# Kernel optimization log

Hardware: AMD Instinct MI355X
Metric: run time of the kernel (lower is better)

## Reference

```python
import jax, jax.numpy as jnp
import numpy as np

B, F, ND, NE = 1024, 1024, 256, 256

def setup_inputs() -> dict:
    key = jax.random.key(0)
    k1, k2, k3 = jax.random.split(key, 3)
    x = jax.random.normal(k1, (B, F), dtype=jnp.float32)
    # xavier-uniform-like init scale for (F+1, units)
    lim_d = float(np.sqrt(6.0 / (F + 1 + ND)))
    lim_e = float(np.sqrt(6.0 / (F + 1 + NE)))
    dilations = jax.random.uniform(k2, (F + 1, ND), minval=-lim_d, maxval=lim_d, dtype=jnp.float32)
    erosions = jax.random.uniform(k3, (F + 1, NE), minval=-lim_e, maxval=lim_e, dtype=jnp.float32)
    return {"x": x, "dilations": dilations, "erosions": erosions}

def reference(x, dilations, erosions):
    b = x.shape[0]
    # append a zero 'bias' feature -> (b, F+1)
    xb = jnp.concatenate([x, jnp.zeros((b, 1), dtype=x.dtype)], axis=1)
    # tropical matmuls: max-plus (dilation), min-minus (erosion)
    dilated = jnp.max(xb[:, :, None] + dilations[None, :, :], axis=1)   # (b, ND)
    eroded = jnp.min(xb[:, :, None] - erosions[None, :, :], axis=1)     # (b, NE)
    return jnp.concatenate([eroded, dilated], axis=1)
```

## Files before the change

### kernel.cpp

```cpp
#include <hip/hip_runtime.h>
#include <math.h>

#define BB   1024
#define FF   1024
#define NOUT 512
#define NW   256
#define BT   128
#define NT   64
#define KT   32

__global__ __launch_bounds__(256, 2) void trop_main(
    const float* __restrict__ x,
    const float* __restrict__ dil,
    const float* __restrict__ ero,
    float* __restrict__ dst,
    int ks, int ch, int direct)
{
    const int bx = blockIdx.x;
    const int by = blockIdx.y;
    const int bz = blockIdx.z;
    const bool is_ero = (bx < (NW / NT));
    const float* __restrict__ w = is_ero ? ero : dil;
    const int c0w = is_ero ? bx * NT : bx * NT - NW;
    const int r0 = by * BT;
    const float sgn = is_ero ? -1.0f : 1.0f;

    __shared__ float lds_x[KT][BT];
    __shared__ float lds_w[KT][NT];

    const int tid = threadIdx.x;
    const int cg = tid & 7;
    const int rg = tid >> 3;

    float acc[4][8];
#pragma unroll
    for (int i = 0; i < 4; ++i)
#pragma unroll
        for (int j = 0; j < 8; ++j) acc[i][j] = -INFINITY;

    const int fstart = bz * ch;
    const int nchunk = ch / KT;

    for (int kc = 0; kc < nchunk; ++kc) {
        const int fb = fstart + kc * KT;

#pragma unroll
        for (int it = 0; it < 4; ++it) {
            const int tt = tid + it * 256;
            const int r = tt & 127;
            const int g = tt >> 7;
            const float4 v = *(const float4*)(x + (size_t)(r0 + r) * FF + fb + g * 4);
            lds_x[g * 4 + 0][r] = sgn * v.x;
            lds_x[g * 4 + 1][r] = sgn * v.y;
            lds_x[g * 4 + 2][r] = sgn * v.z;
            lds_x[g * 4 + 3][r] = sgn * v.w;
        }
#pragma unroll
        for (int it = 0; it < 2; ++it) {
            const int tt = tid + it * 256;
            const int f = tt >> 4;
            const int c4 = tt & 15;
            *(float4*)&lds_w[f][c4 * 4] =
                *(const float4*)(w + (size_t)(fb + f) * NW + c0w + c4 * 4);
        }
        __syncthreads();

#pragma unroll
        for (int ff = 0; ff < KT; ff += 2) {
            const float4 x0 = *(const float4*)&lds_x[ff][rg << 2];
            const float4 x1 = *(const float4*)&lds_x[ff + 1][rg << 2];
            const float4 wa0 = *(const float4*)&lds_w[ff][cg << 3];
            const float4 wb0 = *(const float4*)&lds_w[ff][(cg << 3) + 4];
            const float4 wa1 = *(const float4*)&lds_w[ff + 1][cg << 3];
            const float4 wb1 = *(const float4*)&lds_w[ff + 1][(cg << 3) + 4];
            const float xr0[4] = {x0.x, x0.y, x0.z, x0.w};
            const float xr1[4] = {x1.x, x1.y, x1.z, x1.w};
            const float wc0[8] = {wa0.x, wa0.y, wa0.z, wa0.w, wb0.x, wb0.y, wb0.z, wb0.w};
            const float wc1[8] = {wa1.x, wa1.y, wa1.z, wa1.w, wb1.x, wb1.y, wb1.z, wb1.w};
#pragma unroll
            for (int i = 0; i < 4; ++i)
#pragma unroll
                for (int j = 0; j < 8; ++j) {
                    acc[i][j] = fmaxf(acc[i][j],
                                      fmaxf(xr0[i] + wc0[j], xr1[i] + wc1[j]));
                }
        }
        __syncthreads();
    }

    if (bz == ks - 1) {
        const float4 ba = *(const float4*)(w + (size_t)FF * NW + c0w + (cg << 3));
        const float4 bb = *(const float4*)(w + (size_t)FF * NW + c0w + (cg << 3) + 4);
        const float bc[8] = {ba.x, ba.y, ba.z, ba.w, bb.x, bb.y, bb.z, bb.w};
#pragma unroll
        for (int i = 0; i < 4; ++i)
#pragma unroll
            for (int j = 0; j < 8; ++j) acc[i][j] = fmaxf(acc[i][j], bc[j]);
    }

    float* base = direct ? dst : dst + (size_t)bz * (BB * NOUT);
    const int cglob = bx * NT + (cg << 3);
#pragma unroll
    for (int i = 0; i < 4; ++i) {
        const int row = r0 + (rg << 2) + i;
        float4 v0, v1;
        v0.x = sgn * acc[i][0]; v0.y = sgn * acc[i][1];
        v0.z = sgn * acc[i][2]; v0.w = sgn * acc[i][3];
        v1.x = sgn * acc[i][4]; v1.y = sgn * acc[i][5];
        v1.z = sgn * acc[i][6]; v1.w = sgn * acc[i][7];
        *(float4*)(base + (size_t)row * NOUT + cglob) = v0;
        *(float4*)(base + (size_t)row * NOUT + cglob + 4) = v1;
    }
}

__global__ __launch_bounds__(256) void trop_combine(
    const float* __restrict__ ws, float* __restrict__ out, int ks)
{
    const int i4 = blockIdx.x * blockDim.x + threadIdx.x;
    const int col4 = (i4 << 2) & (NOUT - 1);
    const bool ero = col4 < NW;
    const int stride4 = BB * NOUT / 4;
    float4 v = ((const float4*)ws)[i4];
    for (int z = 1; z < ks; ++z) {
        const float4 u = ((const float4*)ws)[(size_t)z * stride4 + i4];
        if (ero) {
            v.x = fminf(v.x, u.x); v.y = fminf(v.y, u.y);
            v.z = fminf(v.z, u.z); v.w = fminf(v.w, u.w);
        } else {
            v.x = fmaxf(v.x, u.x); v.y = fmaxf(v.y, u.y);
            v.z = fmaxf(v.z, u.z); v.w = fmaxf(v.w, u.w);
        }
    }
    ((float4*)out)[i4] = v;
}

extern "C" void kernel_launch(void* const* d_in, const int* in_sizes, int n_in,
                              void* d_out, int out_size, void* d_ws, size_t ws_size,
                              hipStream_t stream) {
    const float* x = (const float*)d_in[0];
    const float* dil = (const float*)d_in[1];
    const float* ero = (const float*)d_in[2];
    float* out = (float*)d_out;

    const size_t outbytes = (size_t)BB * NOUT * sizeof(float);
    int ks = 1;
    if (ws_size >= 8 * outbytes) ks = 8;
    else if (ws_size >= 4 * outbytes) ks = 4;
    else if (ws_size >= 2 * outbytes) ks = 2;

    if (ks > 1) {
        dim3 grid(NOUT / NT, BB / BT, ks);
        trop_main<<<grid, 256, 0, stream>>>(x, dil, ero, (float*)d_ws, ks, FF / ks, 0);
        const int n4 = BB * NOUT / 4;
        trop_combine<<<n4 / 256, 256, 0, stream>>>((const float*)d_ws, out, ks);
    } else {
        dim3 grid(NOUT / NT, BB / BT, 1);
        trop_main<<<grid, 256, 0, stream>>>(x, dil, ero, out, 1, FF, 1);
    }
}
```

Baseline: 91.02 us.

## Double-buffer LDS tiles with register prefetch and template erosion/dilation paths

Adds double-buffered shared-memory tiles: the global loads for the next K chunk go into registers before computing the current chunk and are written to the other buffer afterward, so only one barrier is needed per chunk. The sign multiplication on x is removed by templating the core on erosion vs dilation, computing w - x directly for erosion. This doubles LDS use to about 48KB per block and raises register pressure from the prefetch registers, which may hurt occupancy at 2 blocks per CU.

```diff
diff --git a/kernel.cpp b/kernel.cpp
--- a/kernel.cpp
+++ b/kernel.cpp
@@ -1,36 +1,30 @@
 #include <hip/hip_runtime.h>
 #include <math.h>
 
-#define BB   1024
-#define FF   1024
-#define NOUT 512
-#define NW   256
-#define BT   128
-#define NT   64
-#define KT   32
+#define BB    1024
+#define FF    1024
+#define NOUT  512
+#define NW    256
+#define BT    128
+#define NT    64
+#define KT    32
 
-__global__ __launch_bounds__(256, 2) void trop_main(
+template<bool ERO>
+__device__ __forceinline__ void core(
+    float (* __restrict__ lx)[KT][BT],
+    float (* __restrict__ lw)[KT][NT],
     const float* __restrict__ x,
-    const float* __restrict__ dil,
-    const float* __restrict__ ero,
+    const float* __restrict__ w,
     float* __restrict__ dst,
-    int ks, int ch, int direct)
+    const int c0w, const int ks, const int ch)
 {
-    const int bx = blockIdx.x;
-    const int by = blockIdx.y;
-    const int bz = blockIdx.z;
-    const bool is_ero = (bx < (NW / NT));
-    const float* __restrict__ w = is_ero ? ero : dil;
-    const int c0w = is_ero ? bx * NT : bx * NT - NW;
-    const int r0 = by * BT;
-    const float sgn = is_ero ? -1.0f : 1.0f;
-
-    __shared__ float lds_x[KT][BT];
-    __shared__ float lds_w[KT][NT];
-
     const int tid = threadIdx.x;
-    const int cg = tid & 7;
-    const int rg = tid >> 3;
+    const int cg  = tid & 7;
+    const int rg  = tid >> 3;
+    const int r0  = blockIdx.y * BT;
+    const int bz  = blockIdx.z;
+    const int fstart = bz * ch;
+    const int nchunk = ch / KT;
 
     float acc[4][8];
 #pragma unroll
@@ -38,41 +32,52 @@
 #pragma unroll
         for (int j = 0; j < 8; ++j) acc[i][j] = -INFINITY;
 
-    const int fstart = bz * ch;
-    const int nchunk = ch / KT;
+    float4 xs[4], ws2[2];
 
-    for (int kc = 0; kc < nchunk; ++kc) {
-        const int fb = fstart + kc * KT;
-
+    auto g_load = [&](int fb) {
 #pragma unroll
         for (int it = 0; it < 4; ++it) {
             const int tt = tid + it * 256;
-            const int r = tt & 127;
-            const int g = tt >> 7;
-            const float4 v = *(const float4*)(x + (size_t)(r0 + r) * FF + fb + g * 4);
-            lds_x[g * 4 + 0][r] = sgn * v.x;
-            lds_x[g * 4 + 1][r] = sgn * v.y;
-            lds_x[g * 4 + 2][r] = sgn * v.z;
-            lds_x[g * 4 + 3][r] = sgn * v.w;
+            const int r  = tt & 127;
+            const int g  = tt >> 7;
+            xs[it] = *(const float4*)(x + (size_t)(r0 + r) * FF + fb + g * 4);
         }
 #pragma unroll
         for (int it = 0; it < 2; ++it) {
             const int tt = tid + it * 256;
-            const int f = tt >> 4;
+            const int f  = tt >> 4;
             const int c4 = tt & 15;
-            *(float4*)&lds_w[f][c4 * 4] =
-                *(const float4*)(w + (size_t)(fb + f) * NW + c0w + c4 * 4);
+            ws2[it] = *(const float4*)(w + (size_t)(fb + f) * NW + c0w + c4 * 4);
         }
-        __syncthreads();
-
+    };
+    auto s_write = [&](int b) {
+#pragma unroll
+        for (int it = 0; it < 4; ++it) {
+            const int tt = tid + it * 256;
+            const int r  = tt & 127;
+            const int g  = tt >> 7;
+            lx[b][g * 4 + 0][r] = xs[it].x;
+            lx[b][g * 4 + 1][r] = xs[it].y;
+            lx[b][g * 4 + 2][r] = xs[it].z;
+            lx[b][g * 4 + 3][r] = xs[it].w;
+        }
+#pragma unroll
+        for (int it = 0; it < 2; ++it) {
+            const int tt = tid + it * 256;
+            const int f  = tt >> 4;
+            const int c4 = tt & 15;
+            *(float4*)&lw[b][f][c4 * 4] = ws2[it];
+        }
+    };
+    auto compute = [&](int b) {
 #pragma unroll
         for (int ff = 0; ff < KT; ff += 2) {
-            const float4 x0 = *(const float4*)&lds_x[ff][rg << 2];
-            const float4 x1 = *(const float4*)&lds_x[ff + 1][rg << 2];
-            const float4 wa0 = *(const float4*)&lds_w[ff][cg << 3];
-            const float4 wb0 = *(const float4*)&lds_w[ff][(cg << 3) + 4];
-            const float4 wa1 = *(const float4*)&lds_w[ff + 1][cg << 3];
-            const float4 wb1 = *(const float4*)&lds_w[ff + 1][(cg << 3) + 4];
+            const float4 x0  = *(const float4*)&lx[b][ff][rg << 2];
+            const float4 x1  = *(const float4*)&lx[b][ff + 1][rg << 2];
+            const float4 wa0 = *(const float4*)&lw[b][ff][cg << 3];
+            const float4 wb0 = *(const float4*)&lw[b][ff][(cg << 3) + 4];
+            const float4 wa1 = *(const float4*)&lw[b][ff + 1][cg << 3];
+            const float4 wb1 = *(const float4*)&lw[b][ff + 1][(cg << 3) + 4];
             const float xr0[4] = {x0.x, x0.y, x0.z, x0.w};
             const float xr1[4] = {x1.x, x1.y, x1.z, x1.w};
             const float wc0[8] = {wa0.x, wa0.y, wa0.z, wa0.w, wb0.x, wb0.y, wb0.z, wb0.w};
@@ -81,10 +86,23 @@
             for (int i = 0; i < 4; ++i)
 #pragma unroll
                 for (int j = 0; j < 8; ++j) {
-                    acc[i][j] = fmaxf(acc[i][j],
-                                      fmaxf(xr0[i] + wc0[j], xr1[i] + wc1[j]));
+                    const float t0 = ERO ? (wc0[j] - xr0[i]) : (xr0[i] + wc0[j]);
+                    const float t1 = ERO ? (wc1[j] - xr1[i]) : (xr1[i] + wc1[j]);
+                    acc[i][j] = fmaxf(acc[i][j], fmaxf(t0, t1));
                 }
         }
+    };
+
+    g_load(fstart);
+    s_write(0);
+    __syncthreads();
+
+    for (int kc = 0; kc < nchunk; ++kc) {
+        const int cb = kc & 1;
+        const bool more = (kc + 1) < nchunk;
+        if (more) g_load(fstart + (kc + 1) * KT);
+        compute(cb);
+        if (more) s_write(cb ^ 1);
         __syncthreads();
     }
 
@@ -98,18 +116,39 @@
             for (int j = 0; j < 8; ++j) acc[i][j] = fmaxf(acc[i][j], bc[j]);
     }
 
-    float* base = direct ? dst : dst + (size_t)bz * (BB * NOUT);
-    const int cglob = bx * NT + (cg << 3);
+    const int cglob = blockIdx.x * NT + (cg << 3);
 #pragma unroll
     for (int i = 0; i < 4; ++i) {
         const int row = r0 + (rg << 2) + i;
         float4 v0, v1;
-        v0.x = sgn * acc[i][0]; v0.y = sgn * acc[i][1];
-        v0.z = sgn * acc[i][2]; v0.w = sgn * acc[i][3];
-        v1.x = sgn * acc[i][4]; v1.y = sgn * acc[i][5];
-        v1.z = sgn * acc[i][6]; v1.w = sgn * acc[i][7];
-        *(float4*)(base + (size_t)row * NOUT + cglob) = v0;
-        *(float4*)(base + (size_t)row * NOUT + cglob + 4) = v1;
+        v0.x = ERO ? -acc[i][0] : acc[i][0];
+        v0.y = ERO ? -acc[i][1] : acc[i][1];
+        v0.z = ERO ? -acc[i][2] : acc[i][2];
+        v0.w = ERO ? -acc[i][3] : acc[i][3];
+        v1.x = ERO ? -acc[i][4] : acc[i][4];
+        v1.y = ERO ? -acc[i][5] : acc[i][5];
+        v1.z = ERO ? -acc[i][6] : acc[i][6];
+        v1.w = ERO ? -acc[i][7] : acc[i][7];
+        *(float4*)(dst + (size_t)row * NOUT + cglob)     = v0;
+        *(float4*)(dst + (size_t)row * NOUT + cglob + 4) = v1;
+    }
+}
+
+__global__ __launch_bounds__(256, 2) void trop_main(
+    const float* __restrict__ x,
+    const float* __restrict__ dil,
+    const float* __restrict__ ero,
+    float* __restrict__ dst,
+    const int ks, const int ch, const int direct)
+{
+    __shared__ float lx[2][KT][BT];
+    __shared__ float lw[2][KT][NT];
+    float* base = direct ? dst : dst + (size_t)blockIdx.z * (BB * NOUT);
+    const int bx = blockIdx.x;
+    if (bx < NW / NT) {
+        core<true >(lx, lw, x, ero, base, bx * NT,      ks, ch);
+    } else {
+        core<false>(lx, lw, x, dil, base, bx * NT - NW, ks, ch);
     }
 }
 
@@ -137,14 +176,14 @@
 extern "C" void kernel_launch(void* const* d_in, const int* in_sizes, int n_in,
                               void* d_out, int out_size, void* d_ws, size_t ws_size,
                               hipStream_t stream) {
-    const float* x = (const float*)d_in[0];
+    const float* x   = (const float*)d_in[0];
     const float* dil = (const float*)d_in[1];
     const float* ero = (const float*)d_in[2];
     float* out = (float*)d_out;
 
     const size_t outbytes = (size_t)BB * NOUT * sizeof(float);
     int ks = 1;
-    if (ws_size >= 8 * outbytes) ks = 8;
+    if      (ws_size >= 8 * outbytes) ks = 8;
     else if (ws_size >= 4 * outbytes) ks = 4;
     else if (ws_size >= 2 * outbytes) ks = 2;
 
```

Result: slower. 295.9 us (+225.1%).

## Template erosion/dilation paths, drop sign multiplies, allow 16-way K split

Applied to the files above, without the earlier changes.

Splits the kernel body into a template specialised for erosion or dilation. The erosion path computes w - x directly instead of multiplying x by a sign when staging it into shared memory, and negates only at the final store. It also moves the trailing barrier to the top of the next iteration, saving one sync per block. The host now allows a 16-way feature split when the workspace is large enough, which raises grid parallelism at the cost of more partial-result traffic and a heavier combine pass.

```diff
diff --git a/kernel.cpp b/kernel.cpp
--- a/kernel.cpp
+++ b/kernel.cpp
@@ -9,28 +9,20 @@
 #define NT   64
 #define KT   32
 
-__global__ __launch_bounds__(256, 2) void trop_main(
+template<bool ERO>
+__device__ __forceinline__ void core(
+    float (* __restrict__ lds_x)[BT],
+    float (* __restrict__ lds_w)[NT],
     const float* __restrict__ x,
-    const float* __restrict__ dil,
-    const float* __restrict__ ero,
+    const float* __restrict__ w,
     float* __restrict__ dst,
-    int ks, int ch, int direct)
+    const int c0w, const int ks, const int ch)
 {
-    const int bx = blockIdx.x;
-    const int by = blockIdx.y;
-    const int bz = blockIdx.z;
-    const bool is_ero = (bx < (NW / NT));
-    const float* __restrict__ w = is_ero ? ero : dil;
-    const int c0w = is_ero ? bx * NT : bx * NT - NW;
-    const int r0 = by * BT;
-    const float sgn = is_ero ? -1.0f : 1.0f;
-
-    __shared__ float lds_x[KT][BT];
-    __shared__ float lds_w[KT][NT];
-
     const int tid = threadIdx.x;
-    const int cg = tid & 7;
-    const int rg = tid >> 3;
+    const int cg  = tid & 7;
+    const int rg  = tid >> 3;
+    const int r0  = blockIdx.y * BT;
+    const int bz  = blockIdx.z;
 
     float acc[4][8];
 #pragma unroll
@@ -43,6 +35,7 @@
 
     for (int kc = 0; kc < nchunk; ++kc) {
         const int fb = fstart + kc * KT;
+        if (kc) __syncthreads();
 
 #pragma unroll
         for (int it = 0; it < 4; ++it) {
@@ -50,10 +43,10 @@
             const int r = tt & 127;
             const int g = tt >> 7;
             const float4 v = *(const float4*)(x + (size_t)(r0 + r) * FF + fb + g * 4);
-            lds_x[g * 4 + 0][r] = sgn * v.x;
-            lds_x[g * 4 + 1][r] = sgn * v.y;
-            lds_x[g * 4 + 2][r] = sgn * v.z;
-            lds_x[g * 4 + 3][r] = sgn * v.w;
+            lds_x[g * 4 + 0][r] = v.x;
+            lds_x[g * 4 + 1][r] = v.y;
+            lds_x[g * 4 + 2][r] = v.z;
+            lds_x[g * 4 + 3][r] = v.w;
         }
 #pragma unroll
         for (int it = 0; it < 2; ++it) {
@@ -67,8 +60,8 @@
 
 #pragma unroll
         for (int ff = 0; ff < KT; ff += 2) {
-            const float4 x0 = *(const float4*)&lds_x[ff][rg << 2];
-            const float4 x1 = *(const float4*)&lds_x[ff + 1][rg << 2];
+            const float4 x0  = *(const float4*)&lds_x[ff][rg << 2];
+            const float4 x1  = *(const float4*)&lds_x[ff + 1][rg << 2];
             const float4 wa0 = *(const float4*)&lds_w[ff][cg << 3];
             const float4 wb0 = *(const float4*)&lds_w[ff][(cg << 3) + 4];
             const float4 wa1 = *(const float4*)&lds_w[ff + 1][cg << 3];
@@ -81,11 +74,11 @@
             for (int i = 0; i < 4; ++i)
 #pragma unroll
                 for (int j = 0; j < 8; ++j) {
-                    acc[i][j] = fmaxf(acc[i][j],
-                                      fmaxf(xr0[i] + wc0[j], xr1[i] + wc1[j]));
+                    const float t0 = ERO ? (wc0[j] - xr0[i]) : (xr0[i] + wc0[j]);
+                    const float t1 = ERO ? (wc1[j] - xr1[i]) : (xr1[i] + wc1[j]);
+                    acc[i][j] = fmaxf(acc[i][j], fmaxf(t0, t1));
                 }
         }
-        __syncthreads();
     }
 
     if (bz == ks - 1) {
@@ -98,18 +91,39 @@
             for (int j = 0; j < 8; ++j) acc[i][j] = fmaxf(acc[i][j], bc[j]);
     }
 
-    float* base = direct ? dst : dst + (size_t)bz * (BB * NOUT);
-    const int cglob = bx * NT + (cg << 3);
+    const int cglob = blockIdx.x * NT + (cg << 3);
 #pragma unroll
     for (int i = 0; i < 4; ++i) {
         const int row = r0 + (rg << 2) + i;
         float4 v0, v1;
-        v0.x = sgn * acc[i][0]; v0.y = sgn * acc[i][1];
-        v0.z = sgn * acc[i][2]; v0.w = sgn * acc[i][3];
-        v1.x = sgn * acc[i][4]; v1.y = sgn * acc[i][5];
-        v1.z = sgn * acc[i][6]; v1.w = sgn * acc[i][7];
-        *(float4*)(base + (size_t)row * NOUT + cglob) = v0;
-        *(float4*)(base + (size_t)row * NOUT + cglob + 4) = v1;
+        v0.x = ERO ? -acc[i][0] : acc[i][0];
+        v0.y = ERO ? -acc[i][1] : acc[i][1];
+        v0.z = ERO ? -acc[i][2] : acc[i][2];
+        v0.w = ERO ? -acc[i][3] : acc[i][3];
+        v1.x = ERO ? -acc[i][4] : acc[i][4];
+        v1.y = ERO ? -acc[i][5] : acc[i][5];
+        v1.z = ERO ? -acc[i][6] : acc[i][6];
+        v1.w = ERO ? -acc[i][7] : acc[i][7];
+        *(float4*)(dst + (size_t)row * NOUT + cglob)     = v0;
+        *(float4*)(dst + (size_t)row * NOUT + cglob + 4) = v1;
+    }
+}
+
+__global__ __launch_bounds__(256, 2) void trop_main(
+    const float* __restrict__ x,
+    const float* __restrict__ dil,
+    const float* __restrict__ ero,
+    float* __restrict__ dst,
+    const int ks, const int ch, const int direct)
+{
+    __shared__ float lds_x[KT][BT];
+    __shared__ float lds_w[KT][NT];
+    float* base = direct ? dst : dst + (size_t)blockIdx.z * (BB * NOUT);
+    const int bx = blockIdx.x;
+    if (bx < NW / NT) {
+        core<true >(lds_x, lds_w, x, ero, base, bx * NT,      ks, ch);
+    } else {
+        core<false>(lds_x, lds_w, x, dil, base, bx * NT - NW, ks, ch);
     }
 }
 
@@ -137,16 +151,17 @@
 extern "C" void kernel_launch(void* const* d_in, const int* in_sizes, int n_in,
                               void* d_out, int out_size, void* d_ws, size_t ws_size,
                               hipStream_t stream) {
-    const float* x = (const float*)d_in[0];
+    const float* x   = (const float*)d_in[0];
     const float* dil = (const float*)d_in[1];
     const float* ero = (const float*)d_in[2];
     float* out = (float*)d_out;
 
     const size_t outbytes = (size_t)BB * NOUT * sizeof(float);
     int ks = 1;
-    if (ws_size >= 8 * outbytes) ks = 8;
-    else if (ws_size >= 4 * outbytes) ks = 4;
-    else if (ws_size >= 2 * outbytes) ks = 2;
+    if      (ws_size >= 16 * outbytes) ks = 16;
+    else if (ws_size >=  8 * outbytes) ks = 8;
+    else if (ws_size >=  4 * outbytes) ks = 4;
+    else if (ws_size >=  2 * outbytes) ks = 2;
 
     if (ks > 1) {
         dim3 grid(NOUT / NT, BB / BT, ks);
```

Measured after the change: 94.75 us. 4.1% more time.
